# Optimization experiments

Hardware: AMD Instinct MI355X
Metric: run time of the kernel (lower is better)

The kernel has to match this reference:

```python
import jax, jax.numpy as jnp
import numpy as np

HEADS = 8
WH, WW = 8, 8
DIM = 256
B = 4096
N = WH * WW  # 64


def _rel_index():
    ch, cw = np.meshgrid(np.arange(WH), np.arange(WW), indexing='ij')
    coords = np.stack([ch.ravel(), cw.ravel()])  # (2, N)
    rel = coords[:, :, None] - coords[:, None, :]  # (2, N, N)
    rel = rel.transpose(1, 2, 0)
    rel[:, :, 0] += WH - 1
    rel[:, :, 1] += WW - 1
    rel[:, :, 0] *= 2 * WW - 1
    return jnp.asarray(rel.sum(-1), dtype=jnp.int32)  # (N, N)


def setup_inputs() -> dict:
    key = jax.random.key(0)
    ks = jax.random.split(key, 6)
    x = jax.random.normal(ks[0], (B, N, DIM), dtype=jnp.float32)
    attn_mask = jnp.zeros((1, HEADS, N, N), dtype=jnp.float32)
    w_qkv = jax.random.normal(ks[1], (3 * DIM, DIM), dtype=jnp.float32) * 0.02
    w_proj = jax.random.normal(ks[2], (DIM, DIM), dtype=jnp.float32) * 0.02
    b_proj = jax.random.normal(ks[3], (DIM,), dtype=jnp.float32) * 0.02
    table = jax.random.normal(ks[4], (225, HEADS), dtype=jnp.float32) * 0.02
    return {"x": x, "attn_mask": attn_mask, "w_qkv": w_qkv, "w_proj": w_proj,
            "b_proj": b_proj, "table": table, "rel_index": _rel_index()}


def reference(x, attn_mask, w_qkv, w_proj, b_proj, table, rel_index):
    Bn, Nn, C = x.shape
    hd = C // HEADS
    qkv = (x @ w_qkv.T).reshape(Bn, Nn, 3, HEADS, hd)
    q = qkv[:, :, 0].transpose(0, 2, 1, 3)  # (B,h,N,d)
    k = qkv[:, :, 1].transpose(0, 2, 1, 3)
    v = qkv[:, :, 2].transpose(0, 2, 1, 3)
    scale = 1.0 / jnp.sqrt(jnp.asarray(hd, dtype=x.dtype))
    attn = jnp.einsum('bhnd,bhmd->bhnm', q, k) * scale
    bias = table[rel_index]  # (N,N,h)
    attn = attn + bias.transpose(2, 0, 1)[None] + attn_mask
    attn = jax.nn.softmax(attn, axis=-1)
    out = jnp.einsum('bhnm,bhmd->bhnd', attn, v)
    out = out.transpose(0, 2, 1, 3).reshape(Bn, Nn, C)
    return out @ w_proj.T + b_proj
```

## Files before the change

### kernel.cpp

```cpp
#include <hip/hip_runtime.h>
#include <hip/hip_bf16.h>

#define HEADS 8
#define NTOK 64
#define DIM 256

typedef __attribute__((ext_vector_type(8))) short bf16x8;
typedef __attribute__((ext_vector_type(4))) short bf16x4;
typedef __attribute__((ext_vector_type(4))) float f32x4;
typedef unsigned short u16;

__device__ __forceinline__ u16 f2bf(float f) {
    union { float f; unsigned u; } c; c.f = f;
    unsigned u = c.u;
    unsigned rounded = u + 0x7FFF + ((u >> 16) & 1);
    return (u16)(rounded >> 16);
}

__global__ void prep_kernel(const float* __restrict__ wqkv,
                            const float* __restrict__ wproj,
                            const float* __restrict__ table,
                            const int* __restrict__ rel_index,
                            const float* __restrict__ mask,
                            u16* __restrict__ wq_bf,
                            u16* __restrict__ wp_bf,
                            float* __restrict__ bias) {
    const int NQ = 768 * 256;
    const int NP = 256 * 256;
    const int NB = HEADS * NTOK * NTOK;
    int total = NQ + NP + NB;
    for (int i = blockIdx.x * blockDim.x + threadIdx.x; i < total;
         i += gridDim.x * blockDim.x) {
        if (i < NQ) {
            wq_bf[i] = f2bf(wqkv[i]);
        } else if (i < NQ + NP) {
            wp_bf[i - NQ] = f2bf(wproj[i - NQ]);
        } else {
            int j = i - (NQ + NP);
            int h = j >> 12;
            int nm = j & 4095;
            bias[j] = table[rel_index[nm] * HEADS + h] + mask[j];
        }
    }
}

__launch_bounds__(512, 2)
__global__ void win_attn_kernel(const float* __restrict__ x,
                                const u16* __restrict__ wq_bf,
                                const u16* __restrict__ wp_bf,
                                const float* __restrict__ bias,
                                const float* __restrict__ b_proj,
                                float* __restrict__ out) {
    __shared__ u16 smem[16896];
    const int b = blockIdx.x;
    const int tid = threadIdx.x;
    const int w = tid >> 6;
    const int l = tid & 63;
    const int l16 = l & 15;
    const int lhi = l >> 4;
    const int h = w;

    const u16* rq0 = wq_bf + (h * 32 + l16) * 256;
    const u16* rq1 = rq0 + 16 * 256;
    const u16* rk0 = wq_bf + (256 + h * 32 + l16) * 256;
    const u16* rk1 = rk0 + 16 * 256;
    const u16* rv0 = wq_bf + (512 + h * 32 + l16) * 256;
    const u16* rv1 = rv0 + 16 * 256;

    bf16x8 aq0 = *reinterpret_cast<const bf16x8*>(rq0 + lhi * 8);
    bf16x8 aq1 = *reinterpret_cast<const bf16x8*>(rq1 + lhi * 8);
    bf16x8 ak0 = *reinterpret_cast<const bf16x8*>(rk0 + lhi * 8);
    bf16x8 ak1 = *reinterpret_cast<const bf16x8*>(rk1 + lhi * 8);
    bf16x8 av0 = *reinterpret_cast<const bf16x8*>(rv0 + lhi * 8);
    bf16x8 av1 = *reinterpret_cast<const bf16x8*>(rv1 + lhi * 8);
    bf16x8 bq0 = *reinterpret_cast<const bf16x8*>(rq0 + 32 + lhi * 8);
    bf16x8 bq1 = *reinterpret_cast<const bf16x8*>(rq1 + 32 + lhi * 8);
    bf16x8 bk0 = *reinterpret_cast<const bf16x8*>(rk0 + 32 + lhi * 8);
    bf16x8 bk1 = *reinterpret_cast<const bf16x8*>(rk1 + 32 + lhi * 8);
    bf16x8 bv0 = *reinterpret_cast<const bf16x8*>(rv0 + 32 + lhi * 8);
    bf16x8 bv1 = *reinterpret_cast<const bf16x8*>(rv1 + 32 + lhi * 8);

    const float* xw = x + (size_t)b * (NTOK * DIM);
#pragma unroll
    for (int it = 0; it < 8; ++it) {
        int idx4 = tid + it * 512;
        float4 v = reinterpret_cast<const float4*>(xw)[idx4];
        int row = idx4 >> 6;
        int col = (idx4 & 63) * 4;
        ushort4 o;
        o.x = f2bf(v.x); o.y = f2bf(v.y); o.z = f2bf(v.z); o.w = f2bf(v.w);
        *reinterpret_cast<ushort4*>(&smem[row * 264 + col]) = o;
    }
    __syncthreads();

    f32x4 qacc[2][4], kacc[2][4], vacc[4][2];
    const f32x4 zero = {0.f, 0.f, 0.f, 0.f};
#pragma unroll
    for (int ct = 0; ct < 2; ++ct)
#pragma unroll
        for (int tt = 0; tt < 4; ++tt) {
            qacc[ct][tt] = zero; kacc[ct][tt] = zero; vacc[tt][ct] = zero;
        }

    for (int ks = 0; ks < 8; ++ks) {
        const int k0 = ks * 32 + lhi * 8;
        bf16x8 xf[4];
#pragma unroll
        for (int tt = 0; tt < 4; ++tt)
            xf[tt] = *reinterpret_cast<const bf16x8*>(&smem[(tt * 16 + l16) * 264 + k0]);
        bf16x8 nq0, nq1, nk0, nk1, nv0, nv1;
        if (ks < 6) {
            nq0 = *reinterpret_cast<const bf16x8*>(rq0 + k0 + 64);
            nq1 = *reinterpret_cast<const bf16x8*>(rq1 + k0 + 64);
            nk0 = *reinterpret_cast<const bf16x8*>(rk0 + k0 + 64);
            nk1 = *reinterpret_cast<const bf16x8*>(rk1 + k0 + 64);
            nv0 = *reinterpret_cast<const bf16x8*>(rv0 + k0 + 64);
            nv1 = *reinterpret_cast<const bf16x8*>(rv1 + k0 + 64);
        }
#pragma unroll
        for (int tt = 0; tt < 4; ++tt) {
            qacc[0][tt] = __builtin_amdgcn_mfma_f32_16x16x32_bf16(aq0, xf[tt], qacc[0][tt], 0, 0, 0);
            qacc[1][tt] = __builtin_amdgcn_mfma_f32_16x16x32_bf16(aq1, xf[tt], qacc[1][tt], 0, 0, 0);
            kacc[0][tt] = __builtin_amdgcn_mfma_f32_16x16x32_bf16(ak0, xf[tt], kacc[0][tt], 0, 0, 0);
            kacc[1][tt] = __builtin_amdgcn_mfma_f32_16x16x32_bf16(ak1, xf[tt], kacc[1][tt], 0, 0, 0);
            vacc[tt][0] = __builtin_amdgcn_mfma_f32_16x16x32_bf16(xf[tt], av0, vacc[tt][0], 0, 0, 0);
            vacc[tt][1] = __builtin_amdgcn_mfma_f32_16x16x32_bf16(xf[tt], av1, vacc[tt][1], 0, 0, 0);
        }
        aq0 = bq0; aq1 = bq1; ak0 = bk0; ak1 = bk1; av0 = bv0; av1 = bv1;
        bq0 = nq0; bq1 = nq1; bk0 = nk0; bk1 = nk1; bv0 = nv0; bv1 = nv1;
    }
    __syncthreads();

    bf16x4 qf[4][2], kf[4][2], vf[4][2];
#pragma unroll
    for (int tt = 0; tt < 4; ++tt)
#pragma unroll
        for (int ct = 0; ct < 2; ++ct) {
            bf16x4 q, k, v;
#pragma unroll
            for (int r = 0; r < 4; ++r) {
                q[r] = (short)f2bf(qacc[ct][tt][r]);
                k[r] = (short)f2bf(kacc[ct][tt][r]);
                v[r] = (short)f2bf(vacc[tt][ct][r]);
            }
            qf[tt][ct] = q; kf[tt][ct] = k; vf[tt][ct] = v;
        }

    {
        const float scale = 0.17677669529663687f;
        const float* biash = bias + h * 4096;
        f32x4 bias_c[4], bias_n[4];
#pragma unroll
        for (int mt = 0; mt < 4; ++mt)
            bias_c[mt] = *reinterpret_cast<const f32x4*>(
                &biash[l16 * 64 + mt * 16 + lhi * 4]);

#pragma unroll
        for (int nt = 0; nt < 4; ++nt) {
            if (nt < 3) {
#pragma unroll
                for (int mt = 0; mt < 4; ++mt)
                    bias_n[mt] = *reinterpret_cast<const f32x4*>(
                        &biash[((nt + 1) * 16 + l16) * 64 + mt * 16 + lhi * 4]);
            }
            f32x4 sacc[4];
#pragma unroll
            for (int mt = 0; mt < 4; ++mt) {
                sacc[mt] = __builtin_amdgcn_mfma_f32_16x16x16bf16_1k(kf[mt][0], qf[nt][0], zero, 0, 0, 0);
                sacc[mt] = __builtin_amdgcn_mfma_f32_16x16x16bf16_1k(kf[mt][1], qf[nt][1], sacc[mt], 0, 0, 0);
            }
            float p[4][4];
            float sum = 0.f;
#pragma unroll
            for (int mt = 0; mt < 4; ++mt)
#pragma unroll
                for (int r = 0; r < 4; ++r) {
                    p[mt][r] = __expf(sacc[mt][r] * scale + bias_c[mt][r]);
                    sum += p[mt][r];
                }
            sum += __shfl_xor(sum, 16, 64);
            sum += __shfl_xor(sum, 32, 64);
            float inv = 1.0f / sum;
            bf16x4 pf[4];
#pragma unroll
            for (int mt = 0; mt < 4; ++mt) {
                bf16x4 pk;
#pragma unroll
                for (int r = 0; r < 4; ++r) pk[r] = (short)f2bf(p[mt][r]);
                pf[mt] = pk;
            }
            f32x4 oa0 = zero, oa1 = zero;
#pragma unroll
            for (int mt = 0; mt < 4; ++mt) {
                oa0 = __builtin_amdgcn_mfma_f32_16x16x16bf16_1k(vf[mt][0], pf[mt], oa0, 0, 0, 0);
                oa1 = __builtin_amdgcn_mfma_f32_16x16x16bf16_1k(vf[mt][1], pf[mt], oa1, 0, 0, 0);
            }
            {
                ushort4 o0, o1;
                o0.x = f2bf(oa0[0] * inv); o0.y = f2bf(oa0[1] * inv);
                o0.z = f2bf(oa0[2] * inv); o0.w = f2bf(oa0[3] * inv);
                o1.x = f2bf(oa1[0] * inv); o1.y = f2bf(oa1[1] * inv);
                o1.z = f2bf(oa1[2] * inv); o1.w = f2bf(oa1[3] * inv);
                u16* orow = &smem[(nt * 16 + l16) * 264 + h * 32 + lhi * 4];
                *reinterpret_cast<ushort4*>(orow) = o0;
                *reinterpret_cast<ushort4*>(orow + 16) = o1;
            }
            if (nt < 3) {
#pragma unroll
                for (int mt = 0; mt < 4; ++mt) bias_c[mt] = bias_n[mt];
            }
        }
    }
    __syncthreads();

    f32x4 acc3[2][4];
#pragma unroll
    for (int t = 0; t < 2; ++t)
#pragma unroll
        for (int tt = 0; tt < 4; ++tt) acc3[t][tt] = zero;

    const u16* prow0 = wp_bf + (w * 16 + l16) * 256;
    const u16* prow1 = wp_bf + ((w + 8) * 16 + l16) * 256;
    bf16x8 wp0 = *reinterpret_cast<const bf16x8*>(prow0 + lhi * 8);
    bf16x8 wp1 = *reinterpret_cast<const bf16x8*>(prow1 + lhi * 8);
    for (int ks = 0; ks < 8; ++ks) {
        const int k0 = ks * 32 + lhi * 8;
        bf16x8 np0, np1;
        if (ks < 7) {
            np0 = *reinterpret_cast<const bf16x8*>(prow0 + k0 + 32);
            np1 = *reinterpret_cast<const bf16x8*>(prow1 + k0 + 32);
        }
#pragma unroll
        for (int tt = 0; tt < 4; ++tt) {
            bf16x8 of = *reinterpret_cast<const bf16x8*>(&smem[(tt * 16 + l16) * 264 + k0]);
            acc3[0][tt] = __builtin_amdgcn_mfma_f32_16x16x32_bf16(wp0, of, acc3[0][tt], 0, 0, 0);
            acc3[1][tt] = __builtin_amdgcn_mfma_f32_16x16x32_bf16(wp1, of, acc3[1][tt], 0, 0, 0);
        }
        wp0 = np0; wp1 = np1;
    }
    float* outw = out + (size_t)b * (NTOK * DIM);
#pragma unroll
    for (int t = 0; t < 2; ++t) {
        int colb = (w + t * 8) * 16 + lhi * 4;
        float4 bp = *reinterpret_cast<const float4*>(&b_proj[colb]);
#pragma unroll
        for (int tt = 0; tt < 4; ++tt) {
            float4 o;
            o.x = acc3[t][tt][0] + bp.x;
            o.y = acc3[t][tt][1] + bp.y;
            o.z = acc3[t][tt][2] + bp.z;
            o.w = acc3[t][tt][3] + bp.w;
            *reinterpret_cast<float4*>(&outw[(tt * 16 + l16) * 256 + colb]) = o;
        }
    }
}

extern "C" void kernel_launch(void* const* d_in, const int* in_sizes, int n_in,
                              void* d_out, int out_size, void* d_ws, size_t ws_size,
                              hipStream_t stream) {
    const float* x     = (const float*)d_in[0];
    const float* mask  = (const float*)d_in[1];
    const float* wqkv  = (const float*)d_in[2];
    const float* wproj = (const float*)d_in[3];
    const float* bproj = (const float*)d_in[4];
    const float* table = (const float*)d_in[5];
    const int*   relix = (const int*)d_in[6];

    u16*   wq_bf = (u16*)d_ws;
    u16*   wp_bf = wq_bf + 768 * 256;
    float* bias  = (float*)(wp_bf + 256 * 256);

    prep_kernel<<<64, 512, 0, stream>>>(wqkv, wproj, table, relix, mask,
                                        wq_bf, wp_bf, bias);
    win_attn_kernel<<<4096, 512, 0, stream>>>(x, wq_bf, wp_bf, bias, bproj,
                                              (float*)d_out);
}
```

Before: 404.9 us.

## Make attention blocks persistent over 16 windows with double-buffered x prefetch

Each workgroup now processes 16 consecutive windows in a loop, with only 256 blocks launched instead of 4096. The next window's x tile is loaded into registers during the output projection and written to a second LDS buffer, overlapping global loads with MFMA work. The aim is to hide x load latency and amortise block launch cost. In exchange, LDS use doubles to about 66KB per block and the grid shrinks to 256 blocks, which leaves few waves per CU and may expose latency instead of hiding it.

```diff
diff --git a/kernel.cpp b/kernel.cpp
--- a/kernel.cpp
+++ b/kernel.cpp
@@ -51,8 +51,8 @@
                                 const float* __restrict__ bias,
                                 const float* __restrict__ b_proj,
                                 float* __restrict__ out) {
-    __shared__ u16 smem[16896];
-    const int b = blockIdx.x;
+    __shared__ u16 smem[33792];
+    const int bid = blockIdx.x;
     const int tid = threadIdx.x;
     const int w = tid >> 6;
     const int l = tid & 63;
@@ -66,192 +66,227 @@
     const u16* rk1 = rk0 + 16 * 256;
     const u16* rv0 = wq_bf + (512 + h * 32 + l16) * 256;
     const u16* rv1 = rv0 + 16 * 256;
-
-    bf16x8 aq0 = *reinterpret_cast<const bf16x8*>(rq0 + lhi * 8);
-    bf16x8 aq1 = *reinterpret_cast<const bf16x8*>(rq1 + lhi * 8);
-    bf16x8 ak0 = *reinterpret_cast<const bf16x8*>(rk0 + lhi * 8);
-    bf16x8 ak1 = *reinterpret_cast<const bf16x8*>(rk1 + lhi * 8);
-    bf16x8 av0 = *reinterpret_cast<const bf16x8*>(rv0 + lhi * 8);
-    bf16x8 av1 = *reinterpret_cast<const bf16x8*>(rv1 + lhi * 8);
-    bf16x8 bq0 = *reinterpret_cast<const bf16x8*>(rq0 + 32 + lhi * 8);
-    bf16x8 bq1 = *reinterpret_cast<const bf16x8*>(rq1 + 32 + lhi * 8);
-    bf16x8 bk0 = *reinterpret_cast<const bf16x8*>(rk0 + 32 + lhi * 8);
-    bf16x8 bk1 = *reinterpret_cast<const bf16x8*>(rk1 + 32 + lhi * 8);
-    bf16x8 bv0 = *reinterpret_cast<const bf16x8*>(rv0 + 32 + lhi * 8);
-    bf16x8 bv1 = *reinterpret_cast<const bf16x8*>(rv1 + 32 + lhi * 8);
-
-    const float* xw = x + (size_t)b * (NTOK * DIM);
-#pragma unroll
-    for (int it = 0; it < 8; ++it) {
-        int idx4 = tid + it * 512;
-        float4 v = reinterpret_cast<const float4*>(xw)[idx4];
-        int row = idx4 >> 6;
-        int col = (idx4 & 63) * 4;
-        ushort4 o;
-        o.x = f2bf(v.x); o.y = f2bf(v.y); o.z = f2bf(v.z); o.w = f2bf(v.w);
-        *reinterpret_cast<ushort4*>(&smem[row * 264 + col]) = o;
+    const u16* prow0 = wp_bf + (w * 16 + l16) * 256;
+    const u16* prow1 = wp_bf + ((w + 8) * 16 + l16) * 256;
+    const float* biash = bias + h * 4096;
+
+    const f32x4 zero = {0.f, 0.f, 0.f, 0.f};
+    const float scale = 0.17677669529663687f;
+
+    {
+        const float* xw = x + (size_t)(bid * 16) * (NTOK * DIM);
+#pragma unroll
+        for (int it = 0; it < 8; ++it) {
+            int idx4 = tid + it * 512;
+            float4 v = reinterpret_cast<const float4*>(xw)[idx4];
+            int row = idx4 >> 6;
+            int col = (idx4 & 63) * 4;
+            ushort4 o;
+            o.x = f2bf(v.x); o.y = f2bf(v.y); o.z = f2bf(v.z); o.w = f2bf(v.w);
+            *reinterpret_cast<ushort4*>(&smem[row * 264 + col]) = o;
+        }
     }
     __syncthreads();
 
-    f32x4 qacc[2][4], kacc[2][4], vacc[4][2];
-    const f32x4 zero = {0.f, 0.f, 0.f, 0.f};
-#pragma unroll
-    for (int ct = 0; ct < 2; ++ct)
-#pragma unroll
-        for (int tt = 0; tt < 4; ++tt) {
-            qacc[ct][tt] = zero; kacc[ct][tt] = zero; vacc[tt][ct] = zero;
-        }
-
-    for (int ks = 0; ks < 8; ++ks) {
-        const int k0 = ks * 32 + lhi * 8;
-        bf16x8 xf[4];
+    u16* cur = smem;
+    u16* nxt = smem + 16896;
+
+#pragma unroll 1
+    for (int i = 0; i < 16; ++i) {
+        const int win = bid * 16 + i;
+
+        f32x4 qacc[2][4], kacc[2][4], vacc[4][2];
+#pragma unroll
+        for (int ct = 0; ct < 2; ++ct)
+#pragma unroll
+            for (int tt = 0; tt < 4; ++tt) {
+                qacc[ct][tt] = zero; kacc[ct][tt] = zero; vacc[tt][ct] = zero;
+            }
+
+        bf16x8 aq0 = *reinterpret_cast<const bf16x8*>(rq0 + lhi * 8);
+        bf16x8 aq1 = *reinterpret_cast<const bf16x8*>(rq1 + lhi * 8);
+        bf16x8 ak0 = *reinterpret_cast<const bf16x8*>(rk0 + lhi * 8);
+        bf16x8 ak1 = *reinterpret_cast<const bf16x8*>(rk1 + lhi * 8);
+        bf16x8 av0 = *reinterpret_cast<const bf16x8*>(rv0 + lhi * 8);
+        bf16x8 av1 = *reinterpret_cast<const bf16x8*>(rv1 + lhi * 8);
+        bf16x8 bq0 = *reinterpret_cast<const bf16x8*>(rq0 + 32 + lhi * 8);
+        bf16x8 bq1 = *reinterpret_cast<const bf16x8*>(rq1 + 32 + lhi * 8);
+        bf16x8 bk0 = *reinterpret_cast<const bf16x8*>(rk0 + 32 + lhi * 8);
+        bf16x8 bk1 = *reinterpret_cast<const bf16x8*>(rk1 + 32 + lhi * 8);
+        bf16x8 bv0 = *reinterpret_cast<const bf16x8*>(rv0 + 32 + lhi * 8);
+        bf16x8 bv1 = *reinterpret_cast<const bf16x8*>(rv1 + 32 + lhi * 8);
+
+        for (int ks = 0; ks < 8; ++ks) {
+            const int k0 = ks * 32 + lhi * 8;
+            bf16x8 xf[4];
+#pragma unroll
+            for (int tt = 0; tt < 4; ++tt)
+                xf[tt] = *reinterpret_cast<const bf16x8*>(&cur[(tt * 16 + l16) * 264 + k0]);
+            bf16x8 nq0, nq1, nk0, nk1, nv0, nv1;
+            if (ks < 6) {
+                nq0 = *reinterpret_cast<const bf16x8*>(rq0 + k0 + 64);
+                nq1 = *reinterpret_cast<const bf16x8*>(rq1 + k0 + 64);
+                nk0 = *reinterpret_cast<const bf16x8*>(rk0 + k0 + 64);
+                nk1 = *reinterpret_cast<const bf16x8*>(rk1 + k0 + 64);
+                nv0 = *reinterpret_cast<const bf16x8*>(rv0 + k0 + 64);
+                nv1 = *reinterpret_cast<const bf16x8*>(rv1 + k0 + 64);
+            }
+#pragma unroll
+            for (int tt = 0; tt < 4; ++tt) {
+                qacc[0][tt] = __builtin_amdgcn_mfma_f32_16x16x32_bf16(aq0, xf[tt], qacc[0][tt], 0, 0, 0);
+                qacc[1][tt] = __builtin_amdgcn_mfma_f32_16x16x32_bf16(aq1, xf[tt], qacc[1][tt], 0, 0, 0);
+                kacc[0][tt] = __builtin_amdgcn_mfma_f32_16x16x32_bf16(ak0, xf[tt], kacc[0][tt], 0, 0, 0);
+                kacc[1][tt] = __builtin_amdgcn_mfma_f32_16x16x32_bf16(ak1, xf[tt], kacc[1][tt], 0, 0, 0);
+                vacc[tt][0] = __builtin_amdgcn_mfma_f32_16x16x32_bf16(xf[tt], av0, vacc[tt][0], 0, 0, 0);
+                vacc[tt][1] = __builtin_amdgcn_mfma_f32_16x16x32_bf16(xf[tt], av1, vacc[tt][1], 0, 0, 0);
+            }
+            aq0 = bq0; aq1 = bq1; ak0 = bk0; ak1 = bk1; av0 = bv0; av1 = bv1;
+            bq0 = nq0; bq1 = nq1; bk0 = nk0; bk1 = nk1; bv0 = nv0; bv1 = nv1;
+        }
+        __syncthreads();
+
+        bf16x4 qf[4][2], kf[4][2], vf[4][2];
 #pragma unroll
         for (int tt = 0; tt < 4; ++tt)
-            xf[tt] = *reinterpret_cast<const bf16x8*>(&smem[(tt * 16 + l16) * 264 + k0]);
-        bf16x8 nq0, nq1, nk0, nk1, nv0, nv1;
-        if (ks < 6) {
-            nq0 = *reinterpret_cast<const bf16x8*>(rq0 + k0 + 64);
-            nq1 = *reinterpret_cast<const bf16x8*>(rq1 + k0 + 64);
-            nk0 = *reinterpret_cast<const bf16x8*>(rk0 + k0 + 64);
-            nk1 = *reinterpret_cast<const bf16x8*>(rk1 + k0 + 64);
-            nv0 = *reinterpret_cast<const bf16x8*>(rv0 + k0 + 64);
-            nv1 = *reinterpret_cast<const bf16x8*>(rv1 + k0 + 64);
-        }
-#pragma unroll
-        for (int tt = 0; tt < 4; ++tt) {
-            qacc[0][tt] = __builtin_amdgcn_mfma_f32_16x16x32_bf16(aq0, xf[tt], qacc[0][tt], 0, 0, 0);
-            qacc[1][tt] = __builtin_amdgcn_mfma_f32_16x16x32_bf16(aq1, xf[tt], qacc[1][tt], 0, 0, 0);
-            kacc[0][tt] = __builtin_amdgcn_mfma_f32_16x16x32_bf16(ak0, xf[tt], kacc[0][tt], 0, 0, 0);
-            kacc[1][tt] = __builtin_amdgcn_mfma_f32_16x16x32_bf16(ak1, xf[tt], kacc[1][tt], 0, 0, 0);
-            vacc[tt][0] = __builtin_amdgcn_mfma_f32_16x16x32_bf16(xf[tt], av0, vacc[tt][0], 0, 0, 0);
-            vacc[tt][1] = __builtin_amdgcn_mfma_f32_16x16x32_bf16(xf[tt], av1, vacc[tt][1], 0, 0, 0);
-        }
-        aq0 = bq0; aq1 = bq1; ak0 = bk0; ak1 = bk1; av0 = bv0; av1 = bv1;
-        bq0 = nq0; bq1 = nq1; bk0 = nk0; bk1 = nk1; bv0 = nv0; bv1 = nv1;
-    }
-    __syncthreads();
-
-    bf16x4 qf[4][2], kf[4][2], vf[4][2];
-#pragma unroll
-    for (int tt = 0; tt < 4; ++tt)
-#pragma unroll
-        for (int ct = 0; ct < 2; ++ct) {
-            bf16x4 q, k, v;
-#pragma unroll
-            for (int r = 0; r < 4; ++r) {
-                q[r] = (short)f2bf(qacc[ct][tt][r]);
-                k[r] = (short)f2bf(kacc[ct][tt][r]);
-                v[r] = (short)f2bf(vacc[tt][ct][r]);
-            }
-            qf[tt][ct] = q; kf[tt][ct] = k; vf[tt][ct] = v;
-        }
-
-    {
-        const float scale = 0.17677669529663687f;
-        const float* biash = bias + h * 4096;
-        f32x4 bias_c[4], bias_n[4];
-#pragma unroll
-        for (int mt = 0; mt < 4; ++mt)
-            bias_c[mt] = *reinterpret_cast<const f32x4*>(
-                &biash[l16 * 64 + mt * 16 + lhi * 4]);
-
-#pragma unroll
-        for (int nt = 0; nt < 4; ++nt) {
-            if (nt < 3) {
+#pragma unroll
+            for (int ct = 0; ct < 2; ++ct) {
+                bf16x4 q, k, v;
+#pragma unroll
+                for (int r = 0; r < 4; ++r) {
+                    q[r] = (short)f2bf(qacc[ct][tt][r]);
+                    k[r] = (short)f2bf(kacc[ct][tt][r]);
+                    v[r] = (short)f2bf(vacc[tt][ct][r]);
+                }
+                qf[tt][ct] = q; kf[tt][ct] = k; vf[tt][ct] = v;
+            }
+
+        {
+            f32x4 bias_c[4], bias_n[4];
+#pragma unroll
+            for (int mt = 0; mt < 4; ++mt)
+                bias_c[mt] = *reinterpret_cast<const f32x4*>(
+                    &biash[l16 * 64 + mt * 16 + lhi * 4]);
+
+#pragma unroll
+            for (int nt = 0; nt < 4; ++nt) {
+                if (nt < 3) {
+#pragma unroll
+                    for (int mt = 0; mt < 4; ++mt)
+                        bias_n[mt] = *reinterpret_cast<const f32x4*>(
+                            &biash[((nt + 1) * 16 + l16) * 64 + mt * 16 + lhi * 4]);
+                }
+                f32x4 sacc[4];
+#pragma unroll
+                for (int mt = 0; mt < 4; ++mt) {
+                    sacc[mt] = __builtin_amdgcn_mfma_f32_16x16x16bf16_1k(kf[mt][0], qf[nt][0], zero, 0, 0, 0);
+                    sacc[mt] = __builtin_amdgcn_mfma_f32_16x16x16bf16_1k(kf[mt][1], qf[nt][1], sacc[mt], 0, 0, 0);
+                }
+                float p[4][4];
+                float sum = 0.f;
 #pragma unroll
                 for (int mt = 0; mt < 4; ++mt)
-                    bias_n[mt] = *reinterpret_cast<const f32x4*>(
-                        &biash[((nt + 1) * 16 + l16) * 64 + mt * 16 + lhi * 4]);
-            }
-            f32x4 sacc[4];
-#pragma unroll
-            for (int mt = 0; mt < 4; ++mt) {
-                sacc[mt] = __builtin_amdgcn_mfma_f32_16x16x16bf16_1k(kf[mt][0], qf[nt][0], zero, 0, 0, 0);
-                sacc[mt] = __builtin_amdgcn_mfma_f32_16x16x16bf16_1k(kf[mt][1], qf[nt][1], sacc[mt], 0, 0, 0);
-            }
-            float p[4][4];
-            float sum = 0.f;
-#pragma unroll
-            for (int mt = 0; mt < 4; ++mt)
-#pragma unroll
-                for (int r = 0; r < 4; ++r) {
-                    p[mt][r] = __expf(sacc[mt][r] * scale + bias_c[mt][r]);
-                    sum += p[mt][r];
-                }
-            sum += __shfl_xor(sum, 16, 64);
-            sum += __shfl_xor(sum, 32, 64);
-            float inv = 1.0f / sum;
-            bf16x4 pf[4];
-#pragma unroll
-            for (int mt = 0; mt < 4; ++mt) {
-                bf16x4 pk;
-#pragma unroll
-                for (int r = 0; r < 4; ++r) pk[r] = (short)f2bf(p[mt][r]);
-                pf[mt] = pk;
-            }
-            f32x4 oa0 = zero, oa1 = zero;
-#pragma unroll
-            for (int mt = 0; mt < 4; ++mt) {
-                oa0 = __builtin_amdgcn_mfma_f32_16x16x16bf16_1k(vf[mt][0], pf[mt], oa0, 0, 0, 0);
-                oa1 = __builtin_amdgcn_mfma_f32_16x16x16bf16_1k(vf[mt][1], pf[mt], oa1, 0, 0, 0);
-            }
-            {
-                ushort4 o0, o1;
-                o0.x = f2bf(oa0[0] * inv); o0.y = f2bf(oa0[1] * inv);
-                o0.z = f2bf(oa0[2] * inv); o0.w = f2bf(oa0[3] * inv);
-                o1.x = f2bf(oa1[0] * inv); o1.y = f2bf(oa1[1] * inv);
-                o1.z = f2bf(oa1[2] * inv); o1.w = f2bf(oa1[3] * inv);
-                u16* orow = &smem[(nt * 16 + l16) * 264 + h * 32 + lhi * 4];
-                *reinterpret_cast<ushort4*>(orow) = o0;
-                *reinterpret_cast<ushort4*>(orow + 16) = o1;
-            }
-            if (nt < 3) {
-#pragma unroll
-                for (int mt = 0; mt < 4; ++mt) bias_c[mt] = bias_n[mt];
-            }
-        }
-    }
-    __syncthreads();
-
-    f32x4 acc3[2][4];
-#pragma unroll
-    for (int t = 0; t < 2; ++t)
-#pragma unroll
-        for (int tt = 0; tt < 4; ++tt) acc3[t][tt] = zero;
-
-    const u16* prow0 = wp_bf + (w * 16 + l16) * 256;
-    const u16* prow1 = wp_bf + ((w + 8) * 16 + l16) * 256;
-    bf16x8 wp0 = *reinterpret_cast<const bf16x8*>(prow0 + lhi * 8);
-    bf16x8 wp1 = *reinterpret_cast<const bf16x8*>(prow1 + lhi * 8);
-    for (int ks = 0; ks < 8; ++ks) {
-        const int k0 = ks * 32 + lhi * 8;
-        bf16x8 np0, np1;
-        if (ks < 7) {
-            np0 = *reinterpret_cast<const bf16x8*>(prow0 + k0 + 32);
-            np1 = *reinterpret_cast<const bf16x8*>(prow1 + k0 + 32);
-        }
-#pragma unroll
-        for (int tt = 0; tt < 4; ++tt) {
-            bf16x8 of = *reinterpret_cast<const bf16x8*>(&smem[(tt * 16 + l16) * 264 + k0]);
-            acc3[0][tt] = __builtin_amdgcn_mfma_f32_16x16x32_bf16(wp0, of, acc3[0][tt], 0, 0, 0);
-            acc3[1][tt] = __builtin_amdgcn_mfma_f32_16x16x32_bf16(wp1, of, acc3[1][tt], 0, 0, 0);
-        }
-        wp0 = np0; wp1 = np1;
-    }
-    float* outw = out + (size_t)b * (NTOK * DIM);
-#pragma unroll
-    for (int t = 0; t < 2; ++t) {
-        int colb = (w + t * 8) * 16 + lhi * 4;
-        float4 bp = *reinterpret_cast<const float4*>(&b_proj[colb]);
-#pragma unroll
-        for (int tt = 0; tt < 4; ++tt) {
-            float4 o;
-            o.x = acc3[t][tt][0] + bp.x;
-            o.y = acc3[t][tt][1] + bp.y;
-            o.z = acc3[t][tt][2] + bp.z;
-            o.w = acc3[t][tt][3] + bp.w;
-            *reinterpret_cast<float4*>(&outw[(tt * 16 + l16) * 256 + colb]) = o;
-        }
+#pragma unroll
+                    for (int r = 0; r < 4; ++r) {
+                        p[mt][r] = __expf(sacc[mt][r] * scale + bias_c[mt][r]);
+                        sum += p[mt][r];
+                    }
+                sum += __shfl_xor(sum, 16, 64);
+                sum += __shfl_xor(sum, 32, 64);
+                float inv = 1.0f / sum;
+                bf16x4 pf[4];
+#pragma unroll
+                for (int mt = 0; mt < 4; ++mt) {
+                    bf16x4 pk;
+#pragma unroll
+                    for (int r = 0; r < 4; ++r) pk[r] = (short)f2bf(p[mt][r]);
+                    pf[mt] = pk;
+                }
+                f32x4 oa0 = zero, oa1 = zero;
+#pragma unroll
+                for (int mt = 0; mt < 4; ++mt) {
+                    oa0 = __builtin_amdgcn_mfma_f32_16x16x16bf16_1k(vf[mt][0], pf[mt], oa0, 0, 0, 0);
+                    oa1 = __builtin_amdgcn_mfma_f32_16x16x16bf16_1k(vf[mt][1], pf[mt], oa1, 0, 0, 0);
+                }
+                {
+                    ushort4 o0, o1;
+                    o0.x = f2bf(oa0[0] * inv); o0.y = f2bf(oa0[1] * inv);
+                    o0.z = f2bf(oa0[2] * inv); o0.w = f2bf(oa0[3] * inv);
+                    o1.x = f2bf(oa1[0] * inv); o1.y = f2bf(oa1[1] * inv);
+                    o1.z = f2bf(oa1[2] * inv); o1.w = f2bf(oa1[3] * inv);
+                    u16* orow = &cur[(nt * 16 + l16) * 264 + h * 32 + lhi * 4];
+                    *reinterpret_cast<ushort4*>(orow) = o0;
+                    *reinterpret_cast<ushort4*>(orow + 16) = o1;
+                }
+                if (nt < 3) {
+#pragma unroll
+                    for (int mt = 0; mt < 4; ++mt) bias_c[mt] = bias_n[mt];
+                }
+            }
+        }
+        __syncthreads();
+
+        const bool have_next = (i < 15);
+        float4 xs[8];
+        if (have_next) {
+            const float* xn = x + (size_t)(win + 1) * (NTOK * DIM);
+#pragma unroll
+            for (int it = 0; it < 8; ++it)
+                xs[it] = reinterpret_cast<const float4*>(xn)[tid + it * 512];
+        }
+
+        f32x4 acc3[2][4];
+#pragma unroll
+        for (int t = 0; t < 2; ++t)
+#pragma unroll
+            for (int tt = 0; tt < 4; ++tt) acc3[t][tt] = zero;
+
+        bf16x8 wp0 = *reinterpret_cast<const bf16x8*>(prow0 + lhi * 8);
+        bf16x8 wp1 = *reinterpret_cast<const bf16x8*>(prow1 + lhi * 8);
+        for (int ks = 0; ks < 8; ++ks) {
+            const int k0 = ks * 32 + lhi * 8;
+            bf16x8 np0, np1;
+            if (ks < 7) {
+                np0 = *reinterpret_cast<const bf16x8*>(prow0 + k0 + 32);
+                np1 = *reinterpret_cast<const bf16x8*>(prow1 + k0 + 32);
+            }
+#pragma unroll
+            for (int tt = 0; tt < 4; ++tt) {
+                bf16x8 of = *reinterpret_cast<const bf16x8*>(&cur[(tt * 16 + l16) * 264 + k0]);
+                acc3[0][tt] = __builtin_amdgcn_mfma_f32_16x16x32_bf16(wp0, of, acc3[0][tt], 0, 0, 0);
+                acc3[1][tt] = __builtin_amdgcn_mfma_f32_16x16x32_bf16(wp1, of, acc3[1][tt], 0, 0, 0);
+            }
+            wp0 = np0; wp1 = np1;
+        }
+        float* outw = out + (size_t)win * (NTOK * DIM);
+#pragma unroll
+        for (int t = 0; t < 2; ++t) {
+            int colb = (w + t * 8) * 16 + lhi * 4;
+            float4 bp = *reinterpret_cast<const float4*>(&b_proj[colb]);
+#pragma unroll
+            for (int tt = 0; tt < 4; ++tt) {
+                float4 o;
+                o.x = acc3[t][tt][0] + bp.x;
+                o.y = acc3[t][tt][1] + bp.y;
+                o.z = acc3[t][tt][2] + bp.z;
+                o.w = acc3[t][tt][3] + bp.w;
+                *reinterpret_cast<float4*>(&outw[(tt * 16 + l16) * 256 + colb]) = o;
+            }
+        }
+
+        if (have_next) {
+#pragma unroll
+            for (int it = 0; it < 8; ++it) {
+                int idx4 = tid + it * 512;
+                int row = idx4 >> 6;
+                int col = (idx4 & 63) * 4;
+                ushort4 o;
+                o.x = f2bf(xs[it].x); o.y = f2bf(xs[it].y);
+                o.z = f2bf(xs[it].z); o.w = f2bf(xs[it].w);
+                *reinterpret_cast<ushort4*>(&nxt[row * 264 + col]) = o;
+            }
+        }
+        __syncthreads();
+        u16* tmp = cur; cur = nxt; nxt = tmp;
     }
 }
 
@@ -272,6 +307,6 @@
 
     prep_kernel<<<64, 512, 0, stream>>>(wqkv, wproj, table, relix, mask,
                                         wq_bf, wp_bf, bias);
-    win_attn_kernel<<<4096, 512, 0, stream>>>(x, wq_bf, wp_bf, bias, bproj,
-                                              (float*)d_out);
+    win_attn_kernel<<<256, 512, 0, stream>>>(x, wq_bf, wp_bf, bias, bproj,
+                                             (float*)d_out);
 }
```

New measurement: 633.9 us. +56.6%, slower.
